# Optimization experiments

Hardware: AMD Instinct MI355X
Metric: run time of the kernel (lower is better)

Reference implementation:

```python
import jax, jax.numpy as jnp
import numpy as np

N_NODES = 50000
N_EDGES = 800000
H_DIM = 64
N_RELS = 8
N_BASES = 2
N_LAYERS = 2


def setup_inputs() -> dict:
    key = jax.random.key(0)
    ks = jax.random.split(key, 10)
    scale = 1.0 / np.sqrt(H_DIM)
    features = jax.random.normal(ks[0], (N_NODES, H_DIM), dtype=jnp.float32)
    src = jax.random.randint(ks[1], (N_EDGES,), 0, N_NODES, dtype=jnp.int32)
    dst = jax.random.randint(ks[2], (N_EDGES,), 0, N_NODES, dtype=jnp.int32)
    etype = jax.random.randint(ks[3], (N_EDGES,), 0, N_RELS, dtype=jnp.int32)
    # basis weights V: [L, B, H, H], coefficients comp: [L, R, B]
    V = jax.random.normal(ks[4], (N_LAYERS, N_BASES, H_DIM, H_DIM), dtype=jnp.float32) * scale
    comp = jax.random.normal(ks[5], (N_LAYERS, N_RELS, N_BASES), dtype=jnp.float32)
    loop_w = jax.random.normal(ks[6], (N_LAYERS, H_DIM, H_DIM), dtype=jnp.float32) * scale
    layer_bias = jnp.zeros((N_LAYERS, H_DIM), dtype=jnp.float32)
    fc_w = jax.random.normal(ks[7], (1, N_NODES * H_DIM), dtype=jnp.float32) * (1.0 / np.sqrt(N_NODES * H_DIM))
    fc_b = jnp.zeros((1,), dtype=jnp.float32)
    return {
        "features": features, "V": V, "comp": comp, "loop_w": loop_w,
        "layer_bias": layer_bias, "fc_w": fc_w, "fc_b": fc_b,
        "src": src, "dst": dst, "etype": etype,
    }


def reference(features, V, comp, loop_w, layer_bias, fc_w, fc_b, src, dst, etype):
    N, H = features.shape
    L = V.shape[0]
    x = features
    for l in range(L):
        # basis decomposition: project nodes through each basis first (N*B*H, cheap),
        # then mix per-edge with relation coefficients -> avoids per-edge [H,H] weights
        proj = jnp.einsum('ni,bio->nbo', x, V[l])          # [N, B, H]
        msg = jnp.einsum('eb,ebo->eo', comp[l][etype], proj[src])  # [E, H]
        agg = jax.ops.segment_sum(msg, dst, num_segments=N)        # [N, H]
        h = agg + x @ loop_w[l] + layer_bias[l]
        x = jax.nn.relu(h) if l < L - 1 else h
    flat = x.reshape(1, -1)                                # [1, N*H]
    return jax.nn.sigmoid(flat @ fc_w.T + fc_b)            # [1, 1]
```

## Files before the change

### kernel.cpp

```cpp
#include <hip/hip_runtime.h>
#include <hip/hip_bf16.h>
#include <math.h>

#define N_NODES 50000
#define N_EDGES 800000
#define HDIM 64

#define NBUCKET 98
#define BSHIFT  9
#define BCAP    10240

typedef short bf16x8 __attribute__((ext_vector_type(8)));
typedef float f32x4  __attribute__((ext_vector_type(4)));
typedef unsigned short ushort_t;

__device__ __forceinline__ ushort_t f2bf(float f) {
    __hip_bfloat16 b = __float2bfloat16(f);
    return *(ushort_t*)&b;
}
__device__ __forceinline__ void unpack8(uint4 u, float* f) {
    f[0] = __uint_as_float(u.x << 16); f[1] = __uint_as_float(u.x & 0xFFFF0000u);
    f[2] = __uint_as_float(u.y << 16); f[3] = __uint_as_float(u.y & 0xFFFF0000u);
    f[4] = __uint_as_float(u.z << 16); f[5] = __uint_as_float(u.z & 0xFFFF0000u);
    f[6] = __uint_as_float(u.w << 16); f[7] = __uint_as_float(u.w & 0xFFFF0000u);
}

__global__ __launch_bounds__(256) void prep_kernel(
    const float* __restrict__ features, ushort_t* __restrict__ x_bf,
    const float* __restrict__ V, const float* __restrict__ lw,
    ushort_t* __restrict__ Wt, int* __restrict__ bucketFill,
    float* __restrict__ scalar)
{
    const int b = blockIdx.x;
    const int t = threadIdx.x;
    if (b < 3125) {
        const int i = b * 256 + t;
        const float4 v = ((const float4*)features)[i];
        ushort4 o = { f2bf(v.x), f2bf(v.y), f2bf(v.z), f2bf(v.w) };
        *(ushort4*)&x_bf[(size_t)i * 4] = o;
    } else if (b < 3221) {
        const int e = (b - 3125) * 256 + t;
        const int l = e / 12288, r = e % 12288;
        const int n = r / 192, k = r % 192;
        const int sel = k >> 6, i = k & 63;
        const float val = (sel < 2) ? V[l * 8192 + sel * 4096 + i * 64 + n]
                                    : lw[l * 4096 + i * 64 + n];
        Wt[e] = f2bf(val);
    } else {
        if (t < NBUCKET) bucketFill[t] = 0;
        if (t == NBUCKET) scalar[0] = 0.0f;
    }
}

__global__ __launch_bounds__(256) void bucket_scatter(
    const int* __restrict__ src, const int* __restrict__ dst,
    const int* __restrict__ etype, int* __restrict__ bucketFill,
    unsigned int* __restrict__ buf)
{
    __shared__ int cnt[NBUCKET];
    __shared__ int base[NBUCKET];
    const int t = threadIdx.x;
    if (t < NBUCKET) cnt[t] = 0;
    __syncthreads();

    int rank[8], bkt[8];
    unsigned pay[8];
    bool valid[8];
#pragma unroll
    for (int k = 0; k < 8; ++k) {
        const int e = blockIdx.x * 2048 + k * 256 + t;
        valid[k] = (e < N_EDGES);
        if (valid[k]) {
            const int d = dst[e];
            const int b = d >> BSHIFT;
            bkt[k] = b;
            pay[k] = (unsigned)src[e] | ((unsigned)etype[e] << 16)
                   | ((unsigned)(d & 511) << 19);
            rank[k] = atomicAdd(&cnt[b], 1);
        }
    }
    __syncthreads();
    if (t < NBUCKET) base[t] = atomicAdd(&bucketFill[t], cnt[t]);
    __syncthreads();
#pragma unroll
    for (int k = 0; k < 8; ++k) {
        if (valid[k]) {
            const int pos = base[bkt[k]] + rank[k];
            if (pos < BCAP) buf[bkt[k] * BCAP + pos] = pay[k];
        }
    }
}

__global__ __launch_bounds__(256) void bucket_sort(
    const unsigned int* __restrict__ buf, const int* __restrict__ bucketFill,
    unsigned int* __restrict__ edges, int* __restrict__ row_ptr)
{
    __shared__ int hist[512];
    __shared__ int lscan[512];
    __shared__ int cnt2[512];
    __shared__ int sfill[128];
    __shared__ int sbase;
    const int b = blockIdx.x;
    const int t = threadIdx.x;

    hist[t] = 0; hist[t + 256] = 0;
    cnt2[t] = 0; cnt2[t + 256] = 0;
    if (t < NBUCKET) sfill[t] = bucketFill[t];
    else if (t < 128) sfill[t] = 0;
    __syncthreads();

    for (int off = 1; off < 128; off <<= 1) {
        int u = (t >= off && t < 128) ? sfill[t - off] : 0;
        __syncthreads();
        if (t < 128) sfill[t] += u;
        __syncthreads();
    }
    const int cntb = min(bucketFill[b], BCAP);
    if (t == 0) sbase = sfill[b] - bucketFill[b];
    __syncthreads();
    const int bb = sbase;

    for (int i = t; i < cntb; i += 256)
        atomicAdd(&hist[buf[b * BCAP + i] >> 19], 1);
    __syncthreads();

    if (t < 64) {
        int carry = 0;
        for (int c = 0; c < 8; ++c) {
            const int h = hist[c * 64 + t];
            int x = h;
#pragma unroll
            for (int off = 1; off < 64; off <<= 1) {
                int u = __shfl_up(x, off, 64);
                if (t >= off) x += u;
            }
            lscan[c * 64 + t] = carry + x - h;
            carry += __shfl(x, 63, 64);
        }
    }
    __syncthreads();

    const int n0 = b << BSHIFT;
    for (int i = t; i < 512; i += 256) {
        const int g = n0 + i;
        if (g < N_NODES) row_ptr[g] = bb + lscan[i];
    }
    if (b == NBUCKET - 1 && t == 0) row_ptr[N_NODES] = bb + cntb;

    for (int i = t; i < cntb; i += 256) {
        const unsigned p = buf[b * BCAP + i];
        const int d = p >> 19;
        const int r = atomicAdd(&cnt2[d], 1);
        edges[bb + lscan[d] + r] = p & 0x7FFFFu;
    }
}

__global__ __launch_bounds__(256) void aggregate_bf(
    const ushort_t* __restrict__ x,
    const unsigned int* __restrict__ edges,
    const int* __restrict__ row_ptr,
    const float* __restrict__ comp_l,
    ushort_t* __restrict__ y)
{
    const int lane = threadIdx.x & 63;
    const int n    = blockIdx.x * 4 + (threadIdx.x >> 6);
    const int g    = lane >> 3;
    const int fo   = lane & 7;

    const int beg = row_ptr[n];
    const int end = row_ptr[n + 1];

    float a0[8], a1[8];
#pragma unroll
    for (int i = 0; i < 8; ++i) { a0[i] = 0.f; a1[i] = 0.f; }

    for (int j = beg; j < end; j += 16) {
        const int j0 = j + g;
        const int j1 = j + 8 + g;
        const unsigned pk0 = edges[(j0 < end) ? j0 : (end - 1)];
        const unsigned pk1 = edges[(j1 < end) ? j1 : (end - 1)];
        float2 c0 = *(const float2*)&comp_l[(pk0 >> 16) * 2];
        float2 c1 = *(const float2*)&comp_l[(pk1 >> 16) * 2];
        if (j0 >= end) { c0.x = 0.f; c0.y = 0.f; }
        if (j1 >= end) { c1.x = 0.f; c1.y = 0.f; }
        const uint4 u0 = *(const uint4*)&x[(size_t)(pk0 & 0xFFFFu) * 64 + fo * 8];
        const uint4 u1 = *(const uint4*)&x[(size_t)(pk1 & 0xFFFFu) * 64 + fo * 8];
        float f0[8], f1[8];
        unpack8(u0, f0);
        unpack8(u1, f1);
#pragma unroll
        for (int i = 0; i < 8; ++i) {
            a0[i] = fmaf(c0.x, f0[i], a0[i]); a1[i] = fmaf(c0.y, f0[i], a1[i]);
            a0[i] = fmaf(c1.x, f1[i], a0[i]); a1[i] = fmaf(c1.y, f1[i], a1[i]);
        }
    }

#pragma unroll
    for (int m = 8; m <= 32; m <<= 1) {
#pragma unroll
        for (int i = 0; i < 8; ++i) {
            a0[i] += __shfl_xor(a0[i], m, 64);
            a1[i] += __shfl_xor(a1[i], m, 64);
        }
    }

    if (g == 0) {
        uint4 o0, o1;
        o0.x = (unsigned)f2bf(a0[0]) | ((unsigned)f2bf(a0[1]) << 16);
        o0.y = (unsigned)f2bf(a0[2]) | ((unsigned)f2bf(a0[3]) << 16);
        o0.z = (unsigned)f2bf(a0[4]) | ((unsigned)f2bf(a0[5]) << 16);
        o0.w = (unsigned)f2bf(a0[6]) | ((unsigned)f2bf(a0[7]) << 16);
        o1.x = (unsigned)f2bf(a1[0]) | ((unsigned)f2bf(a1[1]) << 16);
        o1.y = (unsigned)f2bf(a1[2]) | ((unsigned)f2bf(a1[3]) << 16);
        o1.z = (unsigned)f2bf(a1[4]) | ((unsigned)f2bf(a1[5]) << 16);
        o1.w = (unsigned)f2bf(a1[6]) | ((unsigned)f2bf(a1[7]) << 16);
        *(uint4*)&y[(size_t)n * 128 + fo * 8]      = o0;
        *(uint4*)&y[(size_t)n * 128 + 64 + fo * 8] = o1;
    }
}

template <bool FUSE>
__global__ __launch_bounds__(256) void mfma_transform(
    const ushort_t* __restrict__ y_bf,
    const ushort_t* __restrict__ x_bf,
    const ushort_t* __restrict__ Wt,
    const float* __restrict__ bias,
    const float* __restrict__ fcw,
    ushort_t* __restrict__ xout,
    float* __restrict__ scalar)
{
    __shared__ __align__(16) ushort_t su[64 * 200];
    __shared__ float sred[4];
    const int t = threadIdx.x;
    const int w = t >> 6;
    const int lane = t & 63;
    const int c16 = lane & 15;
    const int quad = lane >> 4;
    const int tile = blockIdx.x;

    bf16x8 wf[6];
#pragma unroll
    for (int kf = 0; kf < 6; ++kf)
        wf[kf] = *(const bf16x8*)&Wt[(w * 16 + c16) * 192 + kf * 32 + quad * 8];
    const float bv = bias[w * 16 + c16];

#pragma unroll
    for (int k = 0; k < 6; ++k) {
        const int cid = t + 256 * k;
        const int row = cid / 24;
        const int part = cid % 24;
        const int n = tile * 64 + row;
        uint4 v = {0u, 0u, 0u, 0u};
        if (n < N_NODES) {
            v = (part < 16) ? *(const uint4*)&y_bf[(size_t)n * 128 + part * 8]
                            : *(const uint4*)&x_bf[(size_t)n * 64 + (part - 16) * 8];
        }
        *(uint4*)&su[row * 200 + part * 8] = v;
    }
    __syncthreads();

    float fsum = 0.f;
#pragma unroll
    for (int mt = 0; mt < 4; ++mt) {
        f32x4 acc = {bv, bv, bv, bv};
#pragma unroll
        for (int kf = 0; kf < 6; ++kf) {
            const bf16x8 af =
                *(const bf16x8*)&su[(mt * 16 + c16) * 200 + kf * 32 + quad * 8];
            acc = __builtin_amdgcn_mfma_f32_16x16x32_bf16(af, wf[kf], acc, 0, 0, 0);
        }
        const int nodeb = tile * 64 + mt * 16 + quad * 4;
        if (FUSE) {
#pragma unroll
            for (int r = 0; r < 4; ++r) {
                const int n = nodeb + r;
                if (n < N_NODES)
                    fsum += acc[r] * fcw[(size_t)n * 64 + w * 16 + c16];
            }
        } else {
#pragma unroll
            for (int r = 0; r < 4; ++r) {
                const int n = nodeb + r;
                if (n < N_NODES)
                    xout[(size_t)n * 64 + w * 16 + c16] = f2bf(fmaxf(acc[r], 0.f));
            }
        }
    }

    if (FUSE) {
#pragma unroll
        for (int off = 32; off; off >>= 1) fsum += __shfl_down(fsum, off, 64);
        if (lane == 0) sred[w] = fsum;
        __syncthreads();
        if (t == 0) atomicAdd(scalar, sred[0] + sred[1] + sred[2] + sred[3]);
    }
}

__global__ void final_sigmoid(const float* __restrict__ scalar,
                              const float* __restrict__ fcb,
                              float* __restrict__ out)
{
    const float v = scalar[0] + fcb[0];
    out[0] = 1.0f / (1.0f + expf(-v));
}

extern "C" void kernel_launch(void* const* d_in, const int* in_sizes, int n_in,
                              void* d_out, int out_size, void* d_ws, size_t ws_size,
                              hipStream_t stream)
{
    const float* features = (const float*)d_in[0];
    const float* V        = (const float*)d_in[1];
    const float* comp     = (const float*)d_in[2];
    const float* loop_w   = (const float*)d_in[3];
    const float* bias     = (const float*)d_in[4];
    const float* fc_w     = (const float*)d_in[5];
    const float* fc_b     = (const float*)d_in[6];
    const int*   src      = (const int*)d_in[7];
    const int*   dst      = (const int*)d_in[8];
    const int*   etype    = (const int*)d_in[9];
    float* out = (float*)d_out;

    char* ws = (char*)d_ws;
    ushort_t*     y_bf    = (ushort_t*)(ws);
    ushort_t*     x_bf    = (ushort_t*)(ws + 12800000);
    ushort_t*     x1_bf   = (ushort_t*)(ws + 19200000);
    ushort_t*     Wt      = (ushort_t*)(ws + 25600000);
    float*        scalar  = (float*)   (ws + 25649152);
    int*          bucketFill = (int*)  (ws + 25649280);
    int*          row_ptr = (int*)     (ws + 25649792);
    unsigned int* edges   = (unsigned int*)(ws + 25849856);
    unsigned int* buf     = (unsigned int*)(ws + 29049856);

    const int aggBlocks = N_NODES / 4;
    const int mtBlocks  = (N_NODES + 63) / 64;
    const int k1Blocks  = (N_EDGES + 2047) / 2048;

    prep_kernel<<<3222, 256, 0, stream>>>(features, x_bf, V, loop_w, Wt,
                                          bucketFill, scalar);
    bucket_scatter<<<k1Blocks, 256, 0, stream>>>(src, dst, etype, bucketFill, buf);
    bucket_sort<<<NBUCKET, 256, 0, stream>>>(buf, bucketFill, edges, row_ptr);

    aggregate_bf<<<aggBlocks, 256, 0, stream>>>(x_bf, edges, row_ptr, comp, y_bf);
    mfma_transform<false><<<mtBlocks, 256, 0, stream>>>(
        y_bf, x_bf, Wt, bias, nullptr, x1_bf, nullptr);

    aggregate_bf<<<aggBlocks, 256, 0, stream>>>(x1_bf, edges, row_ptr, comp + 16, y_bf);
    mfma_transform<true><<<mtBlocks, 256, 0, stream>>>(
        y_bf, x1_bf, Wt + 12288, bias + 64, fc_w, nullptr, scalar);

    final_sigmoid<<<1, 1, 0, stream>>>(scalar, fc_b, out);
}
```

Measured before the change: 207.8 us.

## Fuse edge aggregation into MFMA transform kernel and fold sigmoid into last block

Merges the gather-aggregate kernel with the MFMA dense transform, so aggregated messages are written straight into shared memory and the y_bf intermediate no longer makes a global round trip. Each wave now handles 16 nodes one after another, with 16 lanes per feature half and 4 edge groups. The final sigmoid kernel is removed and the last block does it, detected through a completion counter. This trades per-node parallelism for one fewer launch and less memory traffic: grid size drops from 12500 aggregation blocks to 782 fused blocks, which may hurt latency hiding for the gathers.

```diff
diff --git a/kernel.cpp b/kernel.cpp
--- a/kernel.cpp
+++ b/kernel.cpp
@@ -18,18 +18,16 @@
     __hip_bfloat16 b = __float2bfloat16(f);
     return *(ushort_t*)&b;
 }
-__device__ __forceinline__ void unpack8(uint4 u, float* f) {
+__device__ __forceinline__ void unpack4(uint2 u, float* f) {
     f[0] = __uint_as_float(u.x << 16); f[1] = __uint_as_float(u.x & 0xFFFF0000u);
     f[2] = __uint_as_float(u.y << 16); f[3] = __uint_as_float(u.y & 0xFFFF0000u);
-    f[4] = __uint_as_float(u.z << 16); f[5] = __uint_as_float(u.z & 0xFFFF0000u);
-    f[6] = __uint_as_float(u.w << 16); f[7] = __uint_as_float(u.w & 0xFFFF0000u);
 }
 
 __global__ __launch_bounds__(256) void prep_kernel(
     const float* __restrict__ features, ushort_t* __restrict__ x_bf,
     const float* __restrict__ V, const float* __restrict__ lw,
     ushort_t* __restrict__ Wt, int* __restrict__ bucketFill,
-    float* __restrict__ scalar)
+    float* __restrict__ scalar, unsigned int* __restrict__ done)
 {
     const int b = blockIdx.x;
     const int t = threadIdx.x;
@@ -48,7 +46,7 @@
         Wt[e] = f2bf(val);
     } else {
         if (t < NBUCKET) bucketFill[t] = 0;
-        if (t == NBUCKET) scalar[0] = 0.0f;
+        if (t == NBUCKET) { scalar[0] = 0.0f; done[0] = 0u; }
     }
 }
 
@@ -155,89 +153,30 @@
     }
 }
 
-__global__ __launch_bounds__(256) void aggregate_bf(
+template <bool FUSE>
+__global__ __launch_bounds__(256) void layer_fused(
     const ushort_t* __restrict__ x,
     const unsigned int* __restrict__ edges,
     const int* __restrict__ row_ptr,
     const float* __restrict__ comp_l,
-    ushort_t* __restrict__ y)
-{
-    const int lane = threadIdx.x & 63;
-    const int n    = blockIdx.x * 4 + (threadIdx.x >> 6);
-    const int g    = lane >> 3;
-    const int fo   = lane & 7;
-
-    const int beg = row_ptr[n];
-    const int end = row_ptr[n + 1];
-
-    float a0[8], a1[8];
-#pragma unroll
-    for (int i = 0; i < 8; ++i) { a0[i] = 0.f; a1[i] = 0.f; }
-
-    for (int j = beg; j < end; j += 16) {
-        const int j0 = j + g;
-        const int j1 = j + 8 + g;
-        const unsigned pk0 = edges[(j0 < end) ? j0 : (end - 1)];
-        const unsigned pk1 = edges[(j1 < end) ? j1 : (end - 1)];
-        float2 c0 = *(const float2*)&comp_l[(pk0 >> 16) * 2];
-        float2 c1 = *(const float2*)&comp_l[(pk1 >> 16) * 2];
-        if (j0 >= end) { c0.x = 0.f; c0.y = 0.f; }
-        if (j1 >= end) { c1.x = 0.f; c1.y = 0.f; }
-        const uint4 u0 = *(const uint4*)&x[(size_t)(pk0 & 0xFFFFu) * 64 + fo * 8];
-        const uint4 u1 = *(const uint4*)&x[(size_t)(pk1 & 0xFFFFu) * 64 + fo * 8];
-        float f0[8], f1[8];
-        unpack8(u0, f0);
-        unpack8(u1, f1);
-#pragma unroll
-        for (int i = 0; i < 8; ++i) {
-            a0[i] = fmaf(c0.x, f0[i], a0[i]); a1[i] = fmaf(c0.y, f0[i], a1[i]);
-            a0[i] = fmaf(c1.x, f1[i], a0[i]); a1[i] = fmaf(c1.y, f1[i], a1[i]);
-        }
-    }
-
-#pragma unroll
-    for (int m = 8; m <= 32; m <<= 1) {
-#pragma unroll
-        for (int i = 0; i < 8; ++i) {
-            a0[i] += __shfl_xor(a0[i], m, 64);
-            a1[i] += __shfl_xor(a1[i], m, 64);
-        }
-    }
-
-    if (g == 0) {
-        uint4 o0, o1;
-        o0.x = (unsigned)f2bf(a0[0]) | ((unsigned)f2bf(a0[1]) << 16);
-        o0.y = (unsigned)f2bf(a0[2]) | ((unsigned)f2bf(a0[3]) << 16);
-        o0.z = (unsigned)f2bf(a0[4]) | ((unsigned)f2bf(a0[5]) << 16);
-        o0.w = (unsigned)f2bf(a0[6]) | ((unsigned)f2bf(a0[7]) << 16);
-        o1.x = (unsigned)f2bf(a1[0]) | ((unsigned)f2bf(a1[1]) << 16);
-        o1.y = (unsigned)f2bf(a1[2]) | ((unsigned)f2bf(a1[3]) << 16);
-        o1.z = (unsigned)f2bf(a1[4]) | ((unsigned)f2bf(a1[5]) << 16);
-        o1.w = (unsigned)f2bf(a1[6]) | ((unsigned)f2bf(a1[7]) << 16);
-        *(uint4*)&y[(size_t)n * 128 + fo * 8]      = o0;
-        *(uint4*)&y[(size_t)n * 128 + 64 + fo * 8] = o1;
-    }
-}
-
-template <bool FUSE>
-__global__ __launch_bounds__(256) void mfma_transform(
-    const ushort_t* __restrict__ y_bf,
-    const ushort_t* __restrict__ x_bf,
     const ushort_t* __restrict__ Wt,
     const float* __restrict__ bias,
     const float* __restrict__ fcw,
     ushort_t* __restrict__ xout,
-    float* __restrict__ scalar)
+    float* __restrict__ scalar,
+    unsigned int* __restrict__ done,
+    const float* __restrict__ fcb,
+    float* __restrict__ out)
 {
     __shared__ __align__(16) ushort_t su[64 * 200];
     __shared__ float sred[4];
     const int t = threadIdx.x;
     const int w = t >> 6;
     const int lane = t & 63;
+    const int tile = blockIdx.x;
+
     const int c16 = lane & 15;
     const int quad = lane >> 4;
-    const int tile = blockIdx.x;
-
     bf16x8 wf[6];
 #pragma unroll
     for (int kf = 0; kf < 6; ++kf)
@@ -245,17 +184,57 @@
     const float bv = bias[w * 16 + c16];
 
 #pragma unroll
-    for (int k = 0; k < 6; ++k) {
-        const int cid = t + 256 * k;
-        const int row = cid / 24;
-        const int part = cid % 24;
+    for (int p = 0; p < 2; ++p) {
+        const int row = w * 16 + p * 8 + (lane >> 3);
         const int n = tile * 64 + row;
         uint4 v = {0u, 0u, 0u, 0u};
-        if (n < N_NODES) {
-            v = (part < 16) ? *(const uint4*)&y_bf[(size_t)n * 128 + part * 8]
-                            : *(const uint4*)&x_bf[(size_t)n * 64 + (part - 16) * 8];
-        }
-        *(uint4*)&su[row * 200 + part * 8] = v;
+        if (n < N_NODES) v = *(const uint4*)&x[(size_t)n * 64 + (lane & 7) * 8];
+        *(uint4*)&su[row * 200 + 128 + (lane & 7) * 8] = v;
+    }
+
+    const int g  = lane >> 4;
+    const int fh = lane & 15;
+    for (int r = 0; r < 16; ++r) {
+        const int row = w * 16 + r;
+        const int n = tile * 64 + row;
+        int beg = 0, end = 0;
+        if (n < N_NODES) { beg = row_ptr[n]; end = row_ptr[n + 1]; }
+        float a0[4] = {0.f, 0.f, 0.f, 0.f};
+        float a1[4] = {0.f, 0.f, 0.f, 0.f};
+        for (int j = beg; j < end; j += 8) {
+            const int j0 = j + g;
+            const int j1 = j + 4 + g;
+            const unsigned pk0 = edges[(j0 < end) ? j0 : (end - 1)];
+            const unsigned pk1 = edges[(j1 < end) ? j1 : (end - 1)];
+            float2 c0 = *(const float2*)&comp_l[((pk0 >> 16) & 7) * 2];
+            float2 c1 = *(const float2*)&comp_l[((pk1 >> 16) & 7) * 2];
+            if (j0 >= end) { c0.x = 0.f; c0.y = 0.f; }
+            if (j1 >= end) { c1.x = 0.f; c1.y = 0.f; }
+            const uint2 u0 = *(const uint2*)&x[(size_t)(pk0 & 0xFFFFu) * 64 + fh * 4];
+            const uint2 u1 = *(const uint2*)&x[(size_t)(pk1 & 0xFFFFu) * 64 + fh * 4];
+            float f0[4], f1[4];
+            unpack4(u0, f0);
+            unpack4(u1, f1);
+#pragma unroll
+            for (int i = 0; i < 4; ++i) {
+                a0[i] = fmaf(c0.x, f0[i], a0[i]); a1[i] = fmaf(c0.y, f0[i], a1[i]);
+                a0[i] = fmaf(c1.x, f1[i], a0[i]); a1[i] = fmaf(c1.y, f1[i], a1[i]);
+            }
+        }
+#pragma unroll
+        for (int m = 16; m <= 32; m <<= 1) {
+#pragma unroll
+            for (int i = 0; i < 4; ++i) {
+                a0[i] += __shfl_xor(a0[i], m, 64);
+                a1[i] += __shfl_xor(a1[i], m, 64);
+            }
+        }
+        if (g == 0) {
+            ushort4 o0 = { f2bf(a0[0]), f2bf(a0[1]), f2bf(a0[2]), f2bf(a0[3]) };
+            ushort4 o1 = { f2bf(a1[0]), f2bf(a1[1]), f2bf(a1[2]), f2bf(a1[3]) };
+            *(ushort4*)&su[row * 200 + fh * 4]      = o0;
+            *(ushort4*)&su[row * 200 + 64 + fh * 4] = o1;
+        }
     }
     __syncthreads();
 
@@ -292,16 +271,16 @@
         for (int off = 32; off; off >>= 1) fsum += __shfl_down(fsum, off, 64);
         if (lane == 0) sred[w] = fsum;
         __syncthreads();
-        if (t == 0) atomicAdd(scalar, sred[0] + sred[1] + sred[2] + sred[3]);
-    }
-}
-
-__global__ void final_sigmoid(const float* __restrict__ scalar,
-                              const float* __restrict__ fcb,
-                              float* __restrict__ out)
-{
-    const float v = scalar[0] + fcb[0];
-    out[0] = 1.0f / (1.0f + expf(-v));
+        if (t == 0) {
+            atomicAdd(scalar, sred[0] + sred[1] + sred[2] + sred[3]);
+            __threadfence();
+            const unsigned old = atomicAdd(done, 1u);
+            if (old == gridDim.x - 1) {
+                const float v = atomicAdd(scalar, 0.0f) + fcb[0];
+                out[0] = 1.0f / (1.0f + expf(-v));
+            }
+        }
+    }
 }
 
 extern "C" void kernel_launch(void* const* d_in, const int* in_sizes, int n_in,
@@ -321,32 +300,29 @@
     float* out = (float*)d_out;
 
     char* ws = (char*)d_ws;
-    ushort_t*     y_bf    = (ushort_t*)(ws);
-    ushort_t*     x_bf    = (ushort_t*)(ws + 12800000);
-    ushort_t*     x1_bf   = (ushort_t*)(ws + 19200000);
-    ushort_t*     Wt      = (ushort_t*)(ws + 25600000);
-    float*        scalar  = (float*)   (ws + 25649152);
-    int*          bucketFill = (int*)  (ws + 25649280);
-    int*          row_ptr = (int*)     (ws + 25649792);
-    unsigned int* edges   = (unsigned int*)(ws + 25849856);
-    unsigned int* buf     = (unsigned int*)(ws + 29049856);
-
-    const int aggBlocks = N_NODES / 4;
-    const int mtBlocks  = (N_NODES + 63) / 64;
-    const int k1Blocks  = (N_EDGES + 2047) / 2048;
+    ushort_t*     x_bf    = (ushort_t*)(ws);
+    ushort_t*     x1_bf   = (ushort_t*)(ws + 6400000);
+    ushort_t*     Wt      = (ushort_t*)(ws + 12800000);
+    float*        scalar  = (float*)   (ws + 12849152);
+    unsigned int* done    = (unsigned int*)(ws + 12849280);
+    int*          bucketFill = (int*)  (ws + 12849408);
+    int*          row_ptr = (int*)     (ws + 12849920);
+    unsigned int* edges   = (unsigned int*)(ws + 13049984);
+    unsigned int* buf     = (unsigned int*)(ws + 16249984);
+
+    const int k1Blocks = (N_EDGES + 2047) / 2048;
+    const int lBlocks  = (N_NODES + 63) / 64;
 
     prep_kernel<<<3222, 256, 0, stream>>>(features, x_bf, V, loop_w, Wt,
-                                          bucketFill, scalar);
+                                          bucketFill, scalar, done);
     bucket_scatter<<<k1Blocks, 256, 0, stream>>>(src, dst, etype, bucketFill, buf);
     bucket_sort<<<NBUCKET, 256, 0, stream>>>(buf, bucketFill, edges, row_ptr);
 
-    aggregate_bf<<<aggBlocks, 256, 0, stream>>>(x_bf, edges, row_ptr, comp, y_bf);
-    mfma_transform<false><<<mtBlocks, 256, 0, stream>>>(
-        y_bf, x_bf, Wt, bias, nullptr, x1_bf, nullptr);
-
-    aggregate_bf<<<aggBlocks, 256, 0, stream>>>(x1_bf, edges, row_ptr, comp + 16, y_bf);
-    mfma_transform<true><<<mtBlocks, 256, 0, stream>>>(
-        y_bf, x1_bf, Wt + 12288, bias + 64, fc_w, nullptr, scalar);
-
-    final_sigmoid<<<1, 1, 0, stream>>>(scalar, fc_b, out);
-}
+    layer_fused<false><<<lBlocks, 256, 0, stream>>>(
+        x_bf, edges, row_ptr, comp, Wt, bias,
+        nullptr, x1_bf, nullptr, nullptr, nullptr, nullptr);
+
+    layer_fused<true><<<lBlocks, 256, 0, stream>>>(
+        x1_bf, edges, row_ptr, comp + 16, Wt + 12288, bias + 64,
+        fc_w, nullptr, scalar, done, fc_b, out);
+}
```

Result: slower. 240.3 us (+15.6%).

## Fuse prep with bucket scatter, give each 8-lane group its own node, fold sigmoid into transform

Applied to the files above, without the earlier changes.

Merges the prep and bucket-scatter kernels into one launch, zeroing the counters with a memset instead. Rewrites aggregation so each group of 8 lanes owns one node and walks its edges serially, removing the cross-group shuffle reduction. Folds the final sigmoid into the last transform through a last-block-done counter. The aggregation change gives up intra-node parallelism and accepts uneven per-node degree within a wave, in exchange for fewer shuffles and less wasted masked work.

```diff
diff --git a/kernel.cpp b/kernel.cpp
--- a/kernel.cpp
+++ b/kernel.cpp
@@ -25,12 +25,16 @@
     f[6] = __uint_as_float(u.w << 16); f[7] = __uint_as_float(u.w & 0xFFFF0000u);
 }
 
-__global__ __launch_bounds__(256) void prep_kernel(
+__global__ __launch_bounds__(256) void prep_scatter(
     const float* __restrict__ features, ushort_t* __restrict__ x_bf,
     const float* __restrict__ V, const float* __restrict__ lw,
-    ushort_t* __restrict__ Wt, int* __restrict__ bucketFill,
-    float* __restrict__ scalar)
-{
+    ushort_t* __restrict__ Wt,
+    const int* __restrict__ src, const int* __restrict__ dst,
+    const int* __restrict__ etype, int* __restrict__ bucketFill,
+    unsigned int* __restrict__ buf)
+{
+    __shared__ int cnt[NBUCKET];
+    __shared__ int base[NBUCKET];
     const int b = blockIdx.x;
     const int t = threadIdx.x;
     if (b < 3125) {
@@ -38,7 +42,9 @@
         const float4 v = ((const float4*)features)[i];
         ushort4 o = { f2bf(v.x), f2bf(v.y), f2bf(v.z), f2bf(v.w) };
         *(ushort4*)&x_bf[(size_t)i * 4] = o;
-    } else if (b < 3221) {
+        return;
+    }
+    if (b < 3221) {
         const int e = (b - 3125) * 256 + t;
         const int l = e / 12288, r = e % 12288;
         const int n = r / 192, k = r % 192;
@@ -46,20 +52,9 @@
         const float val = (sel < 2) ? V[l * 8192 + sel * 4096 + i * 64 + n]
                                     : lw[l * 4096 + i * 64 + n];
         Wt[e] = f2bf(val);
-    } else {
-        if (t < NBUCKET) bucketFill[t] = 0;
-        if (t == NBUCKET) scalar[0] = 0.0f;
-    }
-}
-
-__global__ __launch_bounds__(256) void bucket_scatter(
-    const int* __restrict__ src, const int* __restrict__ dst,
-    const int* __restrict__ etype, int* __restrict__ bucketFill,
-    unsigned int* __restrict__ buf)
-{
-    __shared__ int cnt[NBUCKET];
-    __shared__ int base[NBUCKET];
-    const int t = threadIdx.x;
+        return;
+    }
+    const int blk = b - 3221;
     if (t < NBUCKET) cnt[t] = 0;
     __syncthreads();
 
@@ -68,15 +63,15 @@
     bool valid[8];
 #pragma unroll
     for (int k = 0; k < 8; ++k) {
-        const int e = blockIdx.x * 2048 + k * 256 + t;
+        const int e = blk * 2048 + k * 256 + t;
         valid[k] = (e < N_EDGES);
         if (valid[k]) {
             const int d = dst[e];
-            const int b = d >> BSHIFT;
-            bkt[k] = b;
+            const int bb = d >> BSHIFT;
+            bkt[k] = bb;
             pay[k] = (unsigned)src[e] | ((unsigned)etype[e] << 16)
                    | ((unsigned)(d & 511) << 19);
-            rank[k] = atomicAdd(&cnt[b], 1);
+            rank[k] = atomicAdd(&cnt[bb], 1);
         }
     }
     __syncthreads();
@@ -155,7 +150,7 @@
     }
 }
 
-__global__ __launch_bounds__(256) void aggregate_bf(
+__global__ __launch_bounds__(256) void aggregate2(
     const ushort_t* __restrict__ x,
     const unsigned int* __restrict__ edges,
     const int* __restrict__ row_ptr,
@@ -163,28 +158,27 @@
     ushort_t* __restrict__ y)
 {
     const int lane = threadIdx.x & 63;
-    const int n    = blockIdx.x * 4 + (threadIdx.x >> 6);
-    const int g    = lane >> 3;
-    const int fo   = lane & 7;
-
-    const int beg = row_ptr[n];
-    const int end = row_ptr[n + 1];
+    const int wv   = threadIdx.x >> 6;
+    const int grp  = lane >> 3;
+    const int gl   = lane & 7;
+    const int n    = blockIdx.x * 32 + wv * 8 + grp;
+
+    int beg = 0, end = 0;
+    if (n < N_NODES) { beg = row_ptr[n]; end = row_ptr[n + 1]; }
 
     float a0[8], a1[8];
 #pragma unroll
     for (int i = 0; i < 8; ++i) { a0[i] = 0.f; a1[i] = 0.f; }
 
-    for (int j = beg; j < end; j += 16) {
-        const int j0 = j + g;
-        const int j1 = j + 8 + g;
-        const unsigned pk0 = edges[(j0 < end) ? j0 : (end - 1)];
-        const unsigned pk1 = edges[(j1 < end) ? j1 : (end - 1)];
-        float2 c0 = *(const float2*)&comp_l[(pk0 >> 16) * 2];
-        float2 c1 = *(const float2*)&comp_l[(pk1 >> 16) * 2];
-        if (j0 >= end) { c0.x = 0.f; c0.y = 0.f; }
+    for (int j = beg; j < end; j += 2) {
+        const unsigned pk0 = edges[j];
+        const int j1 = j + 1;
+        const unsigned pk1 = edges[(j1 < end) ? j1 : j];
+        float2 c0 = *(const float2*)&comp_l[((pk0 >> 16) & 7) * 2];
+        float2 c1 = *(const float2*)&comp_l[((pk1 >> 16) & 7) * 2];
         if (j1 >= end) { c1.x = 0.f; c1.y = 0.f; }
-        const uint4 u0 = *(const uint4*)&x[(size_t)(pk0 & 0xFFFFu) * 64 + fo * 8];
-        const uint4 u1 = *(const uint4*)&x[(size_t)(pk1 & 0xFFFFu) * 64 + fo * 8];
+        const uint4 u0 = *(const uint4*)&x[(size_t)(pk0 & 0xFFFFu) * 64 + gl * 8];
+        const uint4 u1 = *(const uint4*)&x[(size_t)(pk1 & 0xFFFFu) * 64 + gl * 8];
         float f0[8], f1[8];
         unpack8(u0, f0);
         unpack8(u1, f1);
@@ -195,16 +189,7 @@
         }
     }
 
-#pragma unroll
-    for (int m = 8; m <= 32; m <<= 1) {
-#pragma unroll
-        for (int i = 0; i < 8; ++i) {
-            a0[i] += __shfl_xor(a0[i], m, 64);
-            a1[i] += __shfl_xor(a1[i], m, 64);
-        }
-    }
-
-    if (g == 0) {
+    if (n < N_NODES) {
         uint4 o0, o1;
         o0.x = (unsigned)f2bf(a0[0]) | ((unsigned)f2bf(a0[1]) << 16);
         o0.y = (unsigned)f2bf(a0[2]) | ((unsigned)f2bf(a0[3]) << 16);
@@ -214,8 +199,8 @@
         o1.y = (unsigned)f2bf(a1[2]) | ((unsigned)f2bf(a1[3]) << 16);
         o1.z = (unsigned)f2bf(a1[4]) | ((unsigned)f2bf(a1[5]) << 16);
         o1.w = (unsigned)f2bf(a1[6]) | ((unsigned)f2bf(a1[7]) << 16);
-        *(uint4*)&y[(size_t)n * 128 + fo * 8]      = o0;
-        *(uint4*)&y[(size_t)n * 128 + 64 + fo * 8] = o1;
+        *(uint4*)&y[(size_t)n * 128 + gl * 8]      = o0;
+        *(uint4*)&y[(size_t)n * 128 + 64 + gl * 8] = o1;
     }
 }
 
@@ -227,7 +212,10 @@
     const float* __restrict__ bias,
     const float* __restrict__ fcw,
     ushort_t* __restrict__ xout,
-    float* __restrict__ scalar)
+    float* __restrict__ scalar,
+    unsigned int* __restrict__ done,
+    const float* __restrict__ fcb,
+    float* __restrict__ out)
 {
     __shared__ __align__(16) ushort_t su[64 * 200];
     __shared__ float sred[4];
@@ -292,16 +280,16 @@
         for (int off = 32; off; off >>= 1) fsum += __shfl_down(fsum, off, 64);
         if (lane == 0) sred[w] = fsum;
         __syncthreads();
-        if (t == 0) atomicAdd(scalar, sred[0] + sred[1] + sred[2] + sred[3]);
-    }
-}
-
-__global__ void final_sigmoid(const float* __restrict__ scalar,
-                              const float* __restrict__ fcb,
-                              float* __restrict__ out)
-{
-    const float v = scalar[0] + fcb[0];
-    out[0] = 1.0f / (1.0f + expf(-v));
+        if (t == 0) {
+            atomicAdd(scalar, sred[0] + sred[1] + sred[2] + sred[3]);
+            __threadfence();
+            const unsigned old = atomicAdd(done, 1u);
+            if (old == gridDim.x - 1) {
+                const float v = atomicAdd(scalar, 0.0f) + fcb[0];
+                out[0] = 1.0f / (1.0f + expf(-v));
+            }
+        }
+    }
 }
 
 extern "C" void kernel_launch(void* const* d_in, const int* in_sizes, int n_in,
@@ -325,28 +313,27 @@
     ushort_t*     x_bf    = (ushort_t*)(ws + 12800000);
     ushort_t*     x1_bf   = (ushort_t*)(ws + 19200000);
     ushort_t*     Wt      = (ushort_t*)(ws + 25600000);
-    float*        scalar  = (float*)   (ws + 25649152);
-    int*          bucketFill = (int*)  (ws + 25649280);
-    int*          row_ptr = (int*)     (ws + 25649792);
+    int*          bucketFill = (int*)  (ws + 25649152);
+    float*        scalar  = (float*)   (ws + 25649552);
+    unsigned int* done    = (unsigned int*)(ws + 25649556);
+    int*          row_ptr = (int*)     (ws + 25649664);
     unsigned int* edges   = (unsigned int*)(ws + 25849856);
     unsigned int* buf     = (unsigned int*)(ws + 29049856);
 
-    const int aggBlocks = N_NODES / 4;
+    hipMemsetAsync(bucketFill, 0, 512, stream);
+
+    const int aggBlocks = (N_NODES + 31) / 32;
     const int mtBlocks  = (N_NODES + 63) / 64;
-    const int k1Blocks  = (N_EDGES + 2047) / 2048;
-
-    prep_kernel<<<3222, 256, 0, stream>>>(features, x_bf, V, loop_w, Wt,
-                                          bucketFill, scalar);
-    bucket_scatter<<<k1Blocks, 256, 0, stream>>>(src, dst, etype, bucketFill, buf);
+
+    prep_scatter<<<3612, 256, 0, stream>>>(features, x_bf, V, loop_w, Wt,
+                                           src, dst, etype, bucketFill, buf);
     bucket_sort<<<NBUCKET, 256, 0, stream>>>(buf, bucketFill, edges, row_ptr);
 
-    aggregate_bf<<<aggBlocks, 256, 0, stream>>>(x_bf, edges, row_ptr, comp, y_bf);
+    aggregate2<<<aggBlocks, 256, 0, stream>>>(x_bf, edges, row_ptr, comp, y_bf);
     mfma_transform<false><<<mtBlocks, 256, 0, stream>>>(
-        y_bf, x_bf, Wt, bias, nullptr, x1_bf, nullptr);
-
-    aggregate_bf<<<aggBlocks, 256, 0, stream>>>(x1_bf, edges, row_ptr, comp + 16, y_bf);
+        y_bf, x_bf, Wt, bias, nullptr, x1_bf, nullptr, nullptr, nullptr, nullptr);
+
+    aggregate2<<<aggBlocks, 256, 0, stream>>>(x1_bf, edges, row_ptr, comp + 16, y_bf);
     mfma_transform<true><<<mtBlocks, 256, 0, stream>>>(
-        y_bf, x1_bf, Wt + 12288, bias + 64, fc_w, nullptr, scalar);
-
-    final_sigmoid<<<1, 1, 0, stream>>>(scalar, fc_b, out);
-}
+        y_bf, x1_bf, Wt + 12288, bias + 64, fc_w, nullptr, scalar, done, fc_b, out);
+}
```

Result: no change. 207.8 us (+0.0%).
